# Optimization experiments

Measured on AMD Instinct MI355X. Metric: run time of the kernel, lower is better.

The kernel has to match this reference:

```python
import jax, jax.numpy as jnp
import numpy as np

# Module config (init_kwargs)
K_PERIODS = 5
PMAX = 512
MIN_PERIOD_THRESHOLD = 2

B, T, N = 32, 2048, 128


def setup_inputs() -> dict:
    key = jax.random.key(0)
    x = jax.random.normal(key, (B, T, N), dtype=jnp.float32)
    return {"x": x}


def reference(x):
    """Faithful dense/padded JAX version of PeriodicityTransform.forward (mask=None).

    The torch module emits ragged PeriodGroups keyed by (cycles, period).
    Since jit requires static shapes, we return the same per-(series, freq)
    information in padded form:
      tiles   : [BN, K, T]  flattened folded tile (row-major cycle x period),
                 zero-padded past take = cycles*periods
      periods : [BN, K] int32
      cycles  : [BN, K] int32
    tiles[bn,k,:take].reshape(cycles, period) equals the torch tile exactly.
    """
    Bq, Tq, Nq = x.shape
    BN = Bq * Nq
    seqs = jnp.transpose(x, (0, 2, 1)).reshape(BN, Tq)  # [BN, T]

    # --- _topk_freq ---
    spec = jnp.fft.rfft(seqs, axis=-1)                   # [BN, T//2+1]
    mag2 = spec.real ** 2 + spec.imag ** 2
    mag2 = mag2.at[..., 0].set(0.0)                      # kill DC
    k = min(K_PERIODS, mag2.shape[-1] - 1)
    _, kidx = jax.lax.top_k(mag2, k)                     # [BN, K]
    kidx = jnp.maximum(kidx, 1).astype(jnp.int32)

    # --- period / cycle computation (valid_lengths == T, no mask) ---
    lengths = jnp.int32(Tq)
    periods = lengths // kidx                            # [BN, K]
    periods = jnp.minimum(periods, PMAX)
    min_period = min(MIN_PERIOD_THRESHOLD, Tq)
    periods = jnp.maximum(periods, min_period)
    periods = jnp.maximum(periods, 1)
    cycles = jnp.maximum(lengths // periods, 1)          # [BN, K]

    take = cycles * periods                              # [BN, K], <= T
    t = jnp.arange(Tq, dtype=jnp.int32)                  # [T]
    start = Tq - take                                    # [BN, K]
    gather_idx = jnp.clip(start[..., None] + t, 0, Tq - 1)  # [BN, K, T]
    valid = t[None, None, :] < take[..., None]           # [BN, K, T]

    src = jnp.broadcast_to(seqs[:, None, :], (BN, k, Tq))
    tiles = jnp.take_along_axis(src, gather_idx, axis=-1)
    tiles = jnp.where(valid, tiles, jnp.zeros((), dtype=tiles.dtype))
    return tiles, periods, cycles
```

## Files before the change

### kernel.cpp

```cpp
#include <hip/hip_runtime.h>

#define B_ 32
#define T_ 2048
#define N_ 128
#define K_ 5
#define BN_ (B_ * N_)
#define PMAX_ 512
#define MINP_ 2

static constexpr double PI_D = 3.14159265358979323846264338327950288;
static constexpr float  S2_F = 0.70710678118654752440f;

typedef float vf4 __attribute__((ext_vector_type(4)));

struct cf { float r, i; };

__device__ __forceinline__ void bf_w(cf& u, cf& v, float wr, float wi) {
    const float tr = v.r * wr - v.i * wi;
    const float ti = v.r * wi + v.i * wr;
    v.r = u.r - tr; v.i = u.i - ti;
    u.r += tr;      u.i += ti;
}
__device__ __forceinline__ void bf_1(cf& u, cf& v) {
    const float tr = v.r, ti = v.i;
    v.r = u.r - tr; v.i = u.i - ti;
    u.r += tr;      u.i += ti;
}
__device__ __forceinline__ void bf_mi(cf& u, cf& v) {
    const float tr = v.i, ti = -v.r;
    v.r = u.r - tr; v.i = u.i - ti;
    u.r += tr;      u.i += ti;
}
__device__ __forceinline__ int sw(int i) { return i ^ ((i >> 5) & 31); }

__global__ __launch_bounds__(256) void pt_twiddle(float2* __restrict__ tw) {
    const int m = blockIdx.x * 256 + threadIdx.x;
    if (m < 1024) {
        double s, c;
        sincos(-2.0 * PI_D * (double)m / 2048.0, &s, &c);
        tw[m] = make_float2((float)c, (float)s);
    }
}

__global__ __launch_bounds__(256, 8) void pt_fft_tiles(const float* __restrict__ x,
                                                       float* __restrict__ out,
                                                       const float2* __restrict__ tw) {
    __shared__ __align__(16) float re[2052];
    __shared__ __align__(16) float im[2052];
    __shared__ int sh_take[2][K_];

    const int i0  = blockIdx.x;
    const int q   = ((i0 & 7) << 8) | (i0 >> 3);
    const int bn0 = q * 2;
    const int b   = bn0 >> 7;
    const int n   = bn0 & 127;
    const int tid = threadIdx.x;

    const float* xp = x + (size_t)b * T_ * N_ + n;
    {
        float2 v[8];
#pragma unroll
        for (int m = 0; m < 8; ++m)
            v[m] = *(const float2*)(xp + (size_t)(tid + 256 * m) * N_);
#pragma unroll
        for (int m = 0; m < 8; ++m) {
            const int t = tid + 256 * m;
            const int p = sw((int)(__brev((unsigned)t) >> 21));
            re[p] = v[m].x;
            im[p] = v[m].y;
        }
    }
    __syncthreads();

    {
        const int base = tid * 8;
        cf E[8];
#pragma unroll
        for (int j = 0; j < 8; ++j) { const int p = sw(base + j); E[j].r = re[p]; E[j].i = im[p]; }
        bf_1(E[0], E[1]); bf_1(E[2], E[3]); bf_1(E[4], E[5]); bf_1(E[6], E[7]);
        bf_1(E[0], E[2]); bf_mi(E[1], E[3]); bf_1(E[4], E[6]); bf_mi(E[5], E[7]);
        bf_1(E[0], E[4]); bf_w(E[1], E[5], S2_F, -S2_F);
        bf_mi(E[2], E[6]); bf_w(E[3], E[7], -S2_F, -S2_F);
#pragma unroll
        for (int j = 0; j < 8; ++j) { const int p = sw(base + j); re[p] = E[j].r; im[p] = E[j].i; }
    }
    __syncthreads();

#pragma unroll
    for (int r = 0; r < 2; ++r) {
        const int s    = 4 + 3 * r;
        const int h    = 1 << (s - 1);
        const int bq   = tid & (h - 1);
        const int g    = tid >> (s - 1);
        const int base = g * 8 * h + bq;
        const float2 w1  = tw[bq << (11 - s)];
        const float2 w2a = tw[bq << (10 - s)];
        const float2 w2b = tw[(bq + h) << (10 - s)];
        const float2 w30 = tw[bq << (9 - s)];
        const float2 w31 = tw[(bq + h) << (9 - s)];
        const float2 w32 = tw[(bq + 2 * h) << (9 - s)];
        const float2 w33 = tw[(bq + 3 * h) << (9 - s)];
        cf E[8];
#pragma unroll
        for (int j = 0; j < 8; ++j) { const int p = sw(base + j * h); E[j].r = re[p]; E[j].i = im[p]; }
        bf_w(E[0], E[1], w1.x, w1.y);   bf_w(E[2], E[3], w1.x, w1.y);
        bf_w(E[4], E[5], w1.x, w1.y);   bf_w(E[6], E[7], w1.x, w1.y);
        bf_w(E[0], E[2], w2a.x, w2a.y); bf_w(E[1], E[3], w2b.x, w2b.y);
        bf_w(E[4], E[6], w2a.x, w2a.y); bf_w(E[5], E[7], w2b.x, w2b.y);
        bf_w(E[0], E[4], w30.x, w30.y); bf_w(E[1], E[5], w31.x, w31.y);
        bf_w(E[2], E[6], w32.x, w32.y); bf_w(E[3], E[7], w33.x, w33.y);
#pragma unroll
        for (int j = 0; j < 8; ++j) { const int p = sw(base + j * h); re[p] = E[j].r; im[p] = E[j].i; }
        __syncthreads();
    }

#pragma unroll
    for (int u = 0; u < 2; ++u) {
        const int bb = tid + 256 * u;
        const float2 wA = tw[bb << 1];
        const float2 wB = tw[bb];
        const float2 wC = tw[bb + 512];
        const int p0 = sw(bb), p1 = sw(bb + 512), p2 = sw(bb + 1024), p3 = sw(bb + 1536);
        cf E0 = {re[p0], im[p0]}, E1 = {re[p1], im[p1]};
        cf E2 = {re[p2], im[p2]}, E3 = {re[p3], im[p3]};
        bf_w(E0, E1, wA.x, wA.y); bf_w(E2, E3, wA.x, wA.y);
        bf_w(E0, E2, wB.x, wB.y); bf_w(E1, E3, wC.x, wC.y);
        re[p0] = E0.r; im[p0] = E0.i; re[p1] = E1.r; im[p1] = E1.i;
        re[p2] = E2.r; im[p2] = E2.i; re[p3] = E3.r; im[p3] = E3.i;
    }
    __syncthreads();

    float magsA[4], magsB[4];
#pragma unroll
    for (int m = 0; m < 4; ++m) {
        const int k  = 1 + tid + 256 * m;
        const int nk = 2048 - k;
        const int pk = sw(k), pn = sw(nk);
        const float zr = re[pk], zi = im[pk];
        const float yr = re[pn], yi = im[pn];
        const float ar = zr + yr, ai = zi - yi;
        const float br = zi + yi, bi = yr - zr;
        magsA[m] = ar * ar + ai * ai;
        magsB[m] = br * br + bi * bi;
    }
    __syncthreads();
#pragma unroll
    for (int m = 0; m < 4; ++m) {
        const int pk = sw(1 + tid + 256 * m);
        re[pk] = magsA[m];
        im[pk] = magsB[m];
    }
    __syncthreads();

    float2 v2[8];
#pragma unroll
    for (int m = 0; m < 8; ++m)
        v2[m] = *(const float2*)(xp + (size_t)(tid + 256 * m) * N_);

    const int wid  = tid >> 6;
    const int lane = tid & 63;
    if (wid < 2) {
        const float* marr = wid ? im : re;
        float mv[16];
#pragma unroll
        for (int j = 0; j < 16; ++j) mv[j] = marr[sw(1 + lane + 64 * j)];
        for (int it = 0; it < K_; ++it) {
            float bestv = -2.0f;
            int   besti = 1 << 30;
#pragma unroll
            for (int j = 0; j < 16; ++j) {
                const int k = 1 + lane + 64 * j;
                if (mv[j] > bestv || (mv[j] == bestv && k < besti)) { bestv = mv[j]; besti = k; }
            }
#pragma unroll
            for (int off = 32; off > 0; off >>= 1) {
                const float v3 = __shfl_down(bestv, off);
                const int   i3 = __shfl_down(besti, off);
                if (v3 > bestv || (v3 == bestv && i3 < besti)) { bestv = v3; besti = i3; }
            }
            const int win = __shfl(besti, 0);
#pragma unroll
            for (int j = 0; j < 16; ++j)
                if (1 + lane + 64 * j == win) mv[j] = -1.0f;
            if (lane == 0) {
                int period = T_ / win;
                if (period > PMAX_) period = PMAX_;
                if (period < MINP_) period = MINP_;
                const int cyc = T_ / period;
                sh_take[wid][it] = (period << 16) | (period * cyc);
            }
        }
    }
    __syncthreads();

    const size_t TILES = (size_t)BN_ * K_ * T_;
    if (tid < 2 * K_) {
        const int s2 = tid / K_, k2 = tid % K_;
        const int pk   = sh_take[s2][k2];
        const int per  = pk >> 16;
        const int take = pk & 0xFFFF;
        out[TILES + (size_t)(bn0 + s2) * K_ + k2]                      = (float)per;
        out[TILES + (size_t)BN_ * K_ + (size_t)(bn0 + s2) * K_ + k2]   = (float)(take / per);
    }

#pragma unroll
    for (int m = 0; m < 8; ++m) {
        const int t = tid + 256 * m;
        re[t] = v2[m].x;
        im[t] = v2[m].y;
    }
    __syncthreads();

    float* rowA = out + (size_t)bn0 * (K_ * T_);
#pragma unroll
    for (int m = 0; m < 20; ++m) {
        const int e  = tid + 256 * m;
        const int s2 = (e >= K_ * (T_ / 4)) ? 1 : 0;
        const int w  = e - s2 * (K_ * (T_ / 4));
        const int k  = w >> 9;
        const int p4 = (w & 511) << 2;
        const int take  = sh_take[s2][k] & 0xFFFF;
        const int start = T_ - take;
        const vf4* sq4 = (const vf4*)(s2 ? im : re);
        const int idx = start + p4;
        int a0 = idx >> 2;
        if (a0 > 511) a0 = 511;
        const int sh = idx & 3;
        const vf4 lo = sq4[a0];
        const vf4 hi = sq4[a0 + 1];
        float r0, r1, r2, r3;
        if (sh == 0)      { r0 = lo.x; r1 = lo.y; r2 = lo.z; r3 = lo.w; }
        else if (sh == 1) { r0 = lo.y; r1 = lo.z; r2 = lo.w; r3 = hi.x; }
        else if (sh == 2) { r0 = lo.z; r1 = lo.w; r2 = hi.x; r3 = hi.y; }
        else              { r0 = lo.w; r1 = hi.x; r2 = hi.y; r3 = hi.z; }
        vf4 vv;
        vv.x = (p4 + 0 < take) ? r0 : 0.0f;
        vv.y = (p4 + 1 < take) ? r1 : 0.0f;
        vv.z = (p4 + 2 < take) ? r2 : 0.0f;
        vv.w = (p4 + 3 < take) ? r3 : 0.0f;
        __builtin_nontemporal_store(vv, (vf4*)(rowA + (size_t)(s2 * K_ + k) * T_ + p4));
    }
}

extern "C" void kernel_launch(void* const* d_in, const int* in_sizes, int n_in,
                              void* d_out, int out_size, void* d_ws, size_t ws_size,
                              hipStream_t stream) {
    const float* x = (const float*)d_in[0];
    float* out = (float*)d_out;
    float2* tw = (float2*)d_ws;

    pt_twiddle<<<dim3(4), dim3(256), 0, stream>>>(tw);
    pt_fft_tiles<<<dim3(BN_ / 2), dim3(256), 0, stream>>>(x, out, tw);
}
```

Before: 237.8 us.

## Split fused FFT/top-k kernel and tile-gather kernel into two launches

```diff
diff --git a/kernel.cpp b/kernel.cpp
--- a/kernel.cpp
+++ b/kernel.cpp
@@ -42,11 +42,12 @@
     }
 }
 
-__global__ __launch_bounds__(256, 8) void pt_fft_tiles(const float* __restrict__ x,
-                                                       float* __restrict__ out,
-                                                       const float2* __restrict__ tw) {
-    __shared__ __align__(16) float re[2052];
-    __shared__ __align__(16) float im[2052];
+__global__ __launch_bounds__(256, 8) void pt_fft(const float* __restrict__ x,
+                                                 float* __restrict__ out,
+                                                 const float2* __restrict__ tw,
+                                                 int* __restrict__ table) {
+    __shared__ float re[2048];
+    __shared__ float im[2048];
     __shared__ int sh_take[2][K_];
 
     const int i0  = blockIdx.x;
@@ -152,11 +153,6 @@
     }
     __syncthreads();
 
-    float2 v2[8];
-#pragma unroll
-    for (int m = 0; m < 8; ++m)
-        v2[m] = *(const float2*)(xp + (size_t)(tid + 256 * m) * N_);
-
     const int wid  = tid >> 6;
     const int lane = tid & 63;
     if (wid < 2) {
@@ -201,13 +197,36 @@
         const int take = pk & 0xFFFF;
         out[TILES + (size_t)(bn0 + s2) * K_ + k2]                      = (float)per;
         out[TILES + (size_t)BN_ * K_ + (size_t)(bn0 + s2) * K_ + k2]   = (float)(take / per);
-    }
-
+        table[(bn0 + s2) * K_ + k2] = pk;
+    }
+}
+
+__global__ __launch_bounds__(256, 8) void pt_tiles(const float* __restrict__ x,
+                                                   float* __restrict__ out,
+                                                   const int* __restrict__ table) {
+    __shared__ __align__(16) float seqA[2052];
+    __shared__ __align__(16) float seqB[2052];
+    __shared__ int sh_take[2][K_];
+
+    const int i0  = blockIdx.x;
+    const int q   = ((i0 & 7) << 8) | (i0 >> 3);
+    const int bn0 = q * 2;
+    const int b   = bn0 >> 7;
+    const int n   = bn0 & 127;
+    const int tid = threadIdx.x;
+
+    const float* xp = x + (size_t)b * T_ * N_ + n;
+    float2 v[8];
+#pragma unroll
+    for (int m = 0; m < 8; ++m)
+        v[m] = *(const float2*)(xp + (size_t)(tid + 256 * m) * N_);
+    if (tid < 2 * K_)
+        sh_take[tid / K_][tid % K_] = table[(bn0 + tid / K_) * K_ + (tid % K_)];
 #pragma unroll
     for (int m = 0; m < 8; ++m) {
         const int t = tid + 256 * m;
-        re[t] = v2[m].x;
-        im[t] = v2[m].y;
+        seqA[t] = v[m].x;
+        seqB[t] = v[m].y;
     }
     __syncthreads();
 
@@ -221,7 +240,7 @@
         const int p4 = (w & 511) << 2;
         const int take  = sh_take[s2][k] & 0xFFFF;
         const int start = T_ - take;
-        const vf4* sq4 = (const vf4*)(s2 ? im : re);
+        const vf4* sq4 = (const vf4*)(s2 ? seqB : seqA);
         const int idx = start + p4;
         int a0 = idx >> 2;
         if (a0 > 511) a0 = 511;
@@ -248,7 +267,9 @@
     const float* x = (const float*)d_in[0];
     float* out = (float*)d_out;
     float2* tw = (float2*)d_ws;
+    int* table = (int*)((char*)d_ws + 8192);
 
     pt_twiddle<<<dim3(4), dim3(256), 0, stream>>>(tw);
-    pt_fft_tiles<<<dim3(BN_ / 2), dim3(256), 0, stream>>>(x, out, tw);
-}
+    pt_fft<<<dim3(BN_ / 2), dim3(256), 0, stream>>>(x, out, tw, table);
+    pt_tiles<<<dim3(BN_ / 2), dim3(256), 0, stream>>>(x, out, table);
+}
```

Result: no change. 234.6 us (-1.4%).
